# Kernel tuning notes

Measured on AMD Instinct MI355X. Metric: run time of the kernel, lower is better.

## Reference

```python
import jax, jax.numpy as jnp
import numpy as np

INTRINSIC_DIM = 3  # all linear dims, no periodic dims
EPS = 1e-10


def _cdist(a, b):
    # Euclidean distance via the expanded form; clamp for numerical safety.
    sq = (jnp.sum(a * a, axis=1)[:, None]
          + jnp.sum(b * b, axis=1)[None, :]
          - 2.0 * (a @ b.T))
    return jnp.sqrt(jnp.maximum(sq, 0.0))


def _thin_plate_kernel(r, dim):
    r_safe = jnp.maximum(r, EPS)
    if dim == 2:
        k = r_safe ** 2 * jnp.log(r_safe)
    else:
        k = r_safe ** (dim - 2) * jnp.log(r_safe)
    return jnp.where(r < EPS, jnp.zeros_like(k), k)


def setup_inputs() -> dict:
    key = jax.random.key(0)
    k1, k2, k3, k4 = jax.random.split(key, 4)
    batch, n, d, amb = 16384, 4096, INTRINSIC_DIM, 3
    m = 1 + d  # constant + one linear term per (non-periodic) dim
    u = jax.random.uniform(k1, (batch, d), dtype=jnp.float32)
    control_points = jax.random.uniform(k2, (n, d), dtype=jnp.float32)
    rbf_weights = jax.random.normal(k3, (n, amb), dtype=jnp.float32)
    poly_coeffs = jax.random.normal(k4, (m, amb), dtype=jnp.float32)
    return {"u": u, "control_points": control_points,
            "rbf_weights": rbf_weights, "poly_coeffs": poly_coeffs}


def reference(u, control_points, rbf_weights, poly_coeffs):
    # K_query: (batch, n) TPS kernel on pairwise Euclidean distances
    dists = _cdist(u, control_points)
    K_query = _thin_plate_kernel(dists, dim=INTRINSIC_DIM)
    # Polynomial matrix: [1, x] over all linear dims -> (batch, 1 + d)
    P_query = jnp.concatenate([jnp.ones((u.shape[0], 1), dtype=u.dtype), u], axis=1)
    return K_query @ rbf_weights + P_query @ poly_coeffs
```

## Files before the change

kernel.cpp:

```cpp
#include <hip/hip_runtime.h>


#define BLK 512
#define NS 8
#define QPT 4
#define QPB 256
#define JCHUNK 512
#define JW (JCHUNK / NS)

__global__ __launch_bounds__(BLK) void tps_kernel(
    const float* __restrict__ u,
    const float* __restrict__ cp,
    const float* __restrict__ w,
    const float* __restrict__ poly,
    float* __restrict__ out,
    int batch, int n)
{
    __shared__ float4 s_a[JCHUNK];
    __shared__ float4 s_b[JCHUNK];
    __shared__ float  s_red[NS][QPB * 3];

    const int tid = threadIdx.x;
    const int j0 = blockIdx.y * JCHUNK;

    {
        const int g = j0 + tid;
        const float cx = cp[g * 3 + 0], cy = cp[g * 3 + 1], cz = cp[g * 3 + 2];
        s_a[tid] = make_float4(-2.f * cx, -2.f * cy, -2.f * cz,
                               fmaf(cx, cx, fmaf(cy, cy, cz * cz)));
        s_b[tid] = make_float4(0.5f * w[g * 3 + 0], 0.5f * w[g * 3 + 1],
                               0.5f * w[g * 3 + 2], 0.f);
    }
    __syncthreads();

    const int lane = tid & 63;
    const int wv   = tid >> 6;

    float ux[QPT], uy[QPT], uz[QPT], usq[QPT];
    float ax[QPT], ay[QPT], az[QPT];
#pragma unroll
    for (int k = 0; k < QPT; ++k) {
        const int q  = blockIdx.x * QPB + k * 64 + lane;
        const int ql = q < batch ? q : batch - 1;
        ux[k] = u[ql * 3 + 0];
        uy[k] = u[ql * 3 + 1];
        uz[k] = u[ql * 3 + 2];
        usq[k] = fmaf(ux[k], ux[k], fmaf(uy[k], uy[k], uz[k] * uz[k]));
        ax[k] = ay[k] = az[k] = 0.f;
    }

    if (blockIdx.y == 0 && wv == 0) {
#pragma unroll
        for (int k = 0; k < QPT; ++k) {
            ax[k] = poly[0] + ux[k] * poly[3] + uy[k] * poly[6] + uz[k] * poly[9];
            ay[k] = poly[1] + ux[k] * poly[4] + uy[k] * poly[7] + uz[k] * poly[10];
            az[k] = poly[2] + ux[k] * poly[5] + uy[k] * poly[8] + uz[k] * poly[11];
        }
    }

    const int jlo = wv * JW;
#pragma unroll 4
    for (int j = jlo; j < jlo + JW; ++j) {
        const float4 A = s_a[j];
        const float4 B = s_b[j];
#pragma unroll
        for (int k = 0; k < QPT; ++k) {
            float r2 = fmaf(A.x, ux[k],
                       fmaf(A.y, uy[k],
                       fmaf(A.z, uz[k], A.w + usq[k])));
            r2 = fmaxf(r2, 1e-30f);
            const int bi = __float_as_int(r2);

            float y = __int_as_float(0x5f3759df - (bi >> 1));
            y = y * fmaf(-0.5f * r2, y * y, 1.5f);
            const float sq = r2 * y;

            const int   e  = (bi - 0x3f3504f3) >> 23;
            const float m  = __int_as_float(bi - (e << 23));
            const float s  = m - 1.0f;
            float t = fmaf(s, 0.2f, -0.25f);
            t = fmaf(s, t, 0.33333334f);
            t = fmaf(s, t, -0.5f);
            t = fmaf(s, t, 1.0f);
            const float g = fmaf((float)e, 0.69314718f, s * t);

            const float kk = sq * g;
            ax[k] = fmaf(kk, B.x, ax[k]);
            ay[k] = fmaf(kk, B.y, ay[k]);
            az[k] = fmaf(kk, B.z, az[k]);
        }
    }

#pragma unroll
    for (int k = 0; k < QPT; ++k) {
        const int base = (k * 64 + lane) * 3;
        s_red[wv][base + 0] = ax[k];
        s_red[wv][base + 1] = ay[k];
        s_red[wv][base + 2] = az[k];
    }
    __syncthreads();

    for (int v = tid; v < QPB * 3; v += BLK) {
        float s = 0.f;
#pragma unroll
        for (int ww = 0; ww < NS; ++ww) s += s_red[ww][v];
        const size_t o = (size_t)blockIdx.x * (QPB * 3) + v;
        if (o < (size_t)batch * 3) atomicAdd(&out[o], s);
    }
}

extern "C" void kernel_launch(void* const* d_in, const int* in_sizes, int n_in,
                              void* d_out, int out_size, void* d_ws, size_t ws_size,
                              hipStream_t stream) {
    const float* u    = (const float*)d_in[0];
    const float* cp   = (const float*)d_in[1];
    const float* w    = (const float*)d_in[2];
    const float* poly = (const float*)d_in[3];
    float* out = (float*)d_out;

    const int batch = in_sizes[0] / 3;
    const int n     = in_sizes[1] / 3;

    hipMemsetAsync(d_out, 0, (size_t)out_size * sizeof(float), stream);

    dim3 block(BLK);
    dim3 grid(batch / QPB, n / JCHUNK);
    tps_kernel<<<grid, block, 0, stream>>>(u, cp, w, poly, out, batch, n);
}
```

Before: 97.26 us.

## Use hardware sqrt/log2 intrinsics and shrink block tiling with occupancy hint

```diff
diff --git a/kernel.cpp b/kernel.cpp
--- a/kernel.cpp
+++ b/kernel.cpp
@@ -1,14 +1,14 @@
 #include <hip/hip_runtime.h>
 
 
-#define BLK 512
-#define NS 8
-#define QPT 4
-#define QPB 256
-#define JCHUNK 512
+#define BLK 256
+#define NS 4
+#define QPT 2
+#define QPB 128
+#define JCHUNK 256
 #define JW (JCHUNK / NS)
 
-__global__ __launch_bounds__(BLK) void tps_kernel(
+__global__ __launch_bounds__(BLK, 8) void tps_kernel(
     const float* __restrict__ u,
     const float* __restrict__ cp,
     const float* __restrict__ w,
@@ -20,6 +20,8 @@
     __shared__ float4 s_b[JCHUNK];
     __shared__ float  s_red[NS][QPB * 3];
 
+    const float C = 0.34657359027997264f;
+
     const int tid = threadIdx.x;
     const int j0 = blockIdx.y * JCHUNK;
 
@@ -28,8 +30,8 @@
         const float cx = cp[g * 3 + 0], cy = cp[g * 3 + 1], cz = cp[g * 3 + 2];
         s_a[tid] = make_float4(-2.f * cx, -2.f * cy, -2.f * cz,
                                fmaf(cx, cx, fmaf(cy, cy, cz * cz)));
-        s_b[tid] = make_float4(0.5f * w[g * 3 + 0], 0.5f * w[g * 3 + 1],
-                               0.5f * w[g * 3 + 2], 0.f);
+        s_b[tid] = make_float4(C * w[g * 3 + 0], C * w[g * 3 + 1],
+                               C * w[g * 3 + 2], 0.f);
     }
     __syncthreads();
 
@@ -40,11 +42,10 @@
     float ax[QPT], ay[QPT], az[QPT];
 #pragma unroll
     for (int k = 0; k < QPT; ++k) {
-        const int q  = blockIdx.x * QPB + k * 64 + lane;
-        const int ql = q < batch ? q : batch - 1;
-        ux[k] = u[ql * 3 + 0];
-        uy[k] = u[ql * 3 + 1];
-        uz[k] = u[ql * 3 + 2];
+        const int q = blockIdx.x * QPB + k * 64 + lane;
+        ux[k] = u[q * 3 + 0];
+        uy[k] = u[q * 3 + 1];
+        uz[k] = u[q * 3 + 2];
         usq[k] = fmaf(ux[k], ux[k], fmaf(uy[k], uy[k], uz[k] * uz[k]));
         ax[k] = ay[k] = az[k] = 0.f;
     }
@@ -69,22 +70,8 @@
                        fmaf(A.y, uy[k],
                        fmaf(A.z, uz[k], A.w + usq[k])));
             r2 = fmaxf(r2, 1e-30f);
-            const int bi = __float_as_int(r2);
-
-            float y = __int_as_float(0x5f3759df - (bi >> 1));
-            y = y * fmaf(-0.5f * r2, y * y, 1.5f);
-            const float sq = r2 * y;
-
-            const int   e  = (bi - 0x3f3504f3) >> 23;
-            const float m  = __int_as_float(bi - (e << 23));
-            const float s  = m - 1.0f;
-            float t = fmaf(s, 0.2f, -0.25f);
-            t = fmaf(s, t, 0.33333334f);
-            t = fmaf(s, t, -0.5f);
-            t = fmaf(s, t, 1.0f);
-            const float g = fmaf((float)e, 0.69314718f, s * t);
-
-            const float kk = sq * g;
+            const float kk = __builtin_amdgcn_sqrtf(r2) *
+                             __builtin_amdgcn_logf(r2);
             ax[k] = fmaf(kk, B.x, ax[k]);
             ay[k] = fmaf(kk, B.y, ay[k]);
             az[k] = fmaf(kk, B.z, az[k]);
@@ -101,11 +88,8 @@
     __syncthreads();
 
     for (int v = tid; v < QPB * 3; v += BLK) {
-        float s = 0.f;
-#pragma unroll
-        for (int ww = 0; ww < NS; ++ww) s += s_red[ww][v];
-        const size_t o = (size_t)blockIdx.x * (QPB * 3) + v;
-        if (o < (size_t)batch * 3) atomicAdd(&out[o], s);
+        float s = s_red[0][v] + s_red[1][v] + s_red[2][v] + s_red[3][v];
+        atomicAdd(&out[(size_t)blockIdx.x * (QPB * 3) + v], s);
     }
 }
 
```

Result: faster. 80.32 us (-17.4%).
